# Performance work log

Measured on AMD Instinct MI355X. Metric: run time of the kernel, lower is better.

Reference implementation:

```python
import jax, jax.numpy as jnp
import numpy as np

D_MODEL = 1024
N_HEADS = 16
DH = D_MODEL // N_HEADS
ROPE_THETA = 10000.0


def rotate_half(u):
    h = u.shape[-1] // 2
    return jnp.concatenate([-u[..., h:], u[..., :h]], axis=-1)


def apply_rope(q, k, cos, sin):
    return q * cos + rotate_half(q) * sin, k * cos + rotate_half(k) * sin


def setup_inputs() -> dict:
    key = jax.random.key(0)
    ks = jax.random.split(key, 6)
    B, S = 2, 2048
    x = jax.random.normal(ks[0], (B, S, D_MODEL), dtype=jnp.float32)
    y = jax.random.normal(ks[1], (B, S, D_MODEL), dtype=jnp.float32)
    wq = 0.01 * jax.random.normal(ks[2], (D_MODEL, D_MODEL), dtype=jnp.float32)
    wk = 0.01 * jax.random.normal(ks[3], (D_MODEL, D_MODEL), dtype=jnp.float32)
    wv = 0.01 * jax.random.normal(ks[4], (D_MODEL, D_MODEL), dtype=jnp.float32)
    wo = 0.01 * jax.random.normal(ks[5], (D_MODEL, D_MODEL), dtype=jnp.float32)
    return {"x": x, "y": y, "wq": wq, "wk": wk, "wv": wv, "wo": wo}


def reference(x, y, wq, wk, wv, wo):
    B, S, D = x.shape
    past_length = 0  # default; kv_cache=None

    Q = x @ wq.T                      # (B,S,D)
    K = y                             # NOTE: K is y un-projected (as in source)
    V = y @ wv.T
    # K1 = x @ wk.T is computed in the source but immediately overwritten
    # by the buggy second apply_rope call -> wk is unused in the output.
    V1 = x @ wo.T

    def heads(t):
        return t.reshape(B, S, N_HEADS, DH).transpose(0, 2, 1, 3)  # (B,H,S,dh)

    q_h, k_h, v_h, v1_h = heads(Q), heads(K), heads(V), heads(V1)

    # RoPE tables (past_length:past_length+S rows of the cache)
    freqs = 1.0 / ROPE_THETA ** (jnp.arange(0, DH, 2, dtype=jnp.float32) / DH)
    emb = jnp.arange(past_length, past_length + S, dtype=jnp.float32)[:, None] * freqs[None, :]
    cos = jnp.concatenate([jnp.cos(emb), jnp.cos(emb)], axis=-1)[None, None]  # (1,1,S,dh)
    sin = jnp.concatenate([jnp.sin(emb), jnp.sin(emb)], axis=-1)[None, None]

    q_h, k_h = apply_rope(q_h, k_h, cos, sin)
    # faithful to source: k1 = rope applied AGAIN to the already-roped k
    _, k1_h = apply_rope(q_h, k_h, cos, sin)

    k_full = jnp.concatenate([k_h, k1_h], axis=2)   # (B,H,2S,dh)
    v_full = jnp.concatenate([v_h, v1_h], axis=2)
    S_full = k_full.shape[2]

    # mask: tril(diagonal=past_length) over (S,S_full), last S cols = eye(S)
    rows = jnp.arange(S)[:, None]
    cols = jnp.arange(S_full)[None, :]
    mask = cols <= rows + past_length
    mask = mask.at[:, -S:].set(jnp.eye(S, dtype=bool))  # (S,S_full)

    scores = jnp.einsum("bhqd,bhkd->bhqk", q_h, k_full) / jnp.sqrt(jnp.asarray(DH, x.dtype))
    scores = jnp.where(mask[None, None], scores, jnp.asarray(-1e30, x.dtype))
    attn = jax.nn.softmax(scores, axis=-1)
    out = jnp.einsum("bhqk,bhkd->bhqd", attn, v_full)
    out = out.transpose(0, 2, 1, 3).reshape(B, S, D)

    k_ret = k_full[:, :, :-S, :]
    return out, k_ret
```

## Files before the change

### kernel.cpp

```cpp
#include <hip/hip_runtime.h>

#define DM 1024
#define NHEADS 16
#define DHEAD 64
#define BB 2
#define SS 2048
#define BH (BB*NHEADS)

typedef __attribute__((ext_vector_type(8))) short short8;
typedef __attribute__((ext_vector_type(4))) float float4v;
typedef unsigned short ushort_t;

#define LN1E4_D32 0.28782313662425572f

static __device__ __forceinline__ unsigned short f2bf(float f) {
    union { float f; unsigned u; } v; v.f = f;
    unsigned r = v.u + 0x7fffu + ((v.u >> 16) & 1u);
    return (unsigned short)(r >> 16);
}
static __device__ __forceinline__ float bf2f(unsigned short u) {
    union { float f; unsigned u; } v; v.u = ((unsigned)u) << 16;
    return v.f;
}
static __device__ __forceinline__ unsigned cvtpk_bf16(float lo, float hi) {
    unsigned r;
    asm("v_cvt_pk_bf16_f32 %0, %1, %2" : "=v"(r) : "v"(lo), "v"(hi));
    return r;
}

static __device__ __forceinline__ void gload16(const ushort_t* g, ushort_t* l) {
    __builtin_amdgcn_global_load_lds(
        (const __attribute__((address_space(1))) void*)g,
        (__attribute__((address_space(3))) void*)l, 16, 0, 0);
}

__global__ __launch_bounds__(256) void prep_kernel(
        const float* __restrict__ x, const float* __restrict__ y,
        const float* __restrict__ wq, const float* __restrict__ wv,
        const float* __restrict__ wo,
        ushort_t* __restrict__ xb, ushort_t* __restrict__ wqb,
        ushort_t* __restrict__ wvb, ushort_t* __restrict__ wob,
        float* __restrict__ kout, ushort_t* __restrict__ khb,
        ushort_t* __restrict__ yb) {
    if (blockIdx.x < 3584) {
        int C = blockIdx.x * 256 + threadIdx.x;
        int c  = C & 511;
        int tl = C >> 9;
        int rb = tl >> 5, kb = tl & 31;
        const float* src; ushort_t* dst; int r0;
        if (rb < 32)      { src = x;  r0 = rb * 128;        dst = xb  + (size_t)tl * 4096; }
        else if (rb < 40) { src = wq; r0 = (rb - 32) * 128; dst = wqb + (size_t)(((rb - 32) * 32) + kb) * 4096; }
        else if (rb < 48) { src = wv; r0 = (rb - 40) * 128; dst = wvb + (size_t)(((rb - 40) * 32) + kb) * 4096; }
        else              { src = wo; r0 = (rb - 48) * 128; dst = wob + (size_t)(((rb - 48) * 32) + kb) * 4096; }
        int row = c >> 2, g = c & 3;
        int kk3 = g ^ ((row >> 1) & 3);
        const float* s = src + (size_t)(r0 + row) * DM + kb * 32 + kk3 * 8;
        float4 a0 = *reinterpret_cast<const float4*>(s);
        float4 a1 = *reinterpret_cast<const float4*>(s + 4);
        short8 v;
        v[0] = (short)f2bf(a0.x); v[1] = (short)f2bf(a0.y);
        v[2] = (short)f2bf(a0.z); v[3] = (short)f2bf(a0.w);
        v[4] = (short)f2bf(a1.x); v[5] = (short)f2bf(a1.y);
        v[6] = (short)f2bf(a1.z); v[7] = (short)f2bf(a1.w);
        *reinterpret_cast<short8*>(dst + c * 8) = v;
        return;
    }
    int t = (blockIdx.x - 3584) * 256 + threadIdx.x;
    int i8 = t & 3;
    int s  = (t >> 2) & (SS - 1);
    int bh = t >> 13;
    int h = bh & (NHEADS - 1), b = bh >> 4;

    const float* yp = y + ((size_t)(b * SS + s)) * DM + h * DHEAD + i8 * 8;
    float4 a0 = *reinterpret_cast<const float4*>(yp);
    float4 a1 = *reinterpret_cast<const float4*>(yp + 4);
    float4 b0 = *reinterpret_cast<const float4*>(yp + 32);
    float4 b1 = *reinterpret_cast<const float4*>(yp + 36);
    float u0[8] = {a0.x, a0.y, a0.z, a0.w, a1.x, a1.y, a1.z, a1.w};
    float u1[8] = {b0.x, b0.y, b0.z, b0.w, b1.x, b1.y, b1.z, b1.w};
    float lo[8], hi[8];
#pragma unroll
    for (int j = 0; j < 8; j++) {
        int i = i8 * 8 + j;
        float freq = __expf(-(float)i * LN1E4_D32);
        float th = (float)s * freq;
        float cv = cosf(th), sv = sinf(th);
        lo[j] = u0[j] * cv - u1[j] * sv;
        hi[j] = u1[j] * cv + u0[j] * sv;
    }
    float* op = kout + ((size_t)bh * SS + s) * DHEAD + i8 * 8;
    *reinterpret_cast<float4*>(op)      = (float4){lo[0], lo[1], lo[2], lo[3]};
    *reinterpret_cast<float4*>(op + 4)  = (float4){lo[4], lo[5], lo[6], lo[7]};
    *reinterpret_cast<float4*>(op + 32) = (float4){hi[0], hi[1], hi[2], hi[3]};
    *reinterpret_cast<float4*>(op + 36) = (float4){hi[4], hi[5], hi[6], hi[7]};

    ushort_t* kb = khb + ((size_t)bh * 32 + (s >> 6)) * 4096 + (s & 63) * 64;
    short8 vlo, vhi;
#pragma unroll
    for (int j = 0; j < 8; j++) { vlo[j] = (short)f2bf(lo[j]); vhi[j] = (short)f2bf(hi[j]); }
    *reinterpret_cast<short8*>(kb + ((i8 ^ (s & 7)) << 3))       = vlo;
    *reinterpret_cast<short8*>(kb + (((i8 + 4) ^ (s & 7)) << 3)) = vhi;

    int rowm = b * SS + s;
    int rowin = rowm & 127, rbm = rowm >> 7;
    int g = i8 ^ ((rowin >> 1) & 3);
    ushort_t* yt = yb + ((size_t)(rbm * 32 + h * 2)) * 4096 + rowin * 32 + (g << 3);
    short8 ulo, uhi;
#pragma unroll
    for (int j = 0; j < 8; j++) { ulo[j] = (short)f2bf(u0[j]); uhi[j] = (short)f2bf(u1[j]); }
    *reinterpret_cast<short8*>(yt)        = ulo;
    *reinterpret_cast<short8*>(yt + 4096) = uhi;
}

__global__ __launch_bounds__(256, 2) void gemm3_kernel(
        const ushort_t* __restrict__ xb, const ushort_t* __restrict__ yb,
        const ushort_t* __restrict__ wqb, const ushort_t* __restrict__ wvb,
        const ushort_t* __restrict__ wob,
        ushort_t* __restrict__ qh, ushort_t* __restrict__ vt, ushort_t* __restrict__ v1h) {
    __shared__ __align__(16) char smem[34816];
    ushort_t* As = (ushort_t*)smem;
    ushort_t* Bs = (ushort_t*)(smem + 16384);
    ushort_t (*Ct)[136] = (ushort_t(*)[136])smem;

    int bid = blockIdx.x;
    int xcd = bid & 7;
    int s_  = bid >> 3;
    int zo  = s_ >> 5;
    int z   = (zo == 0) ? 0 : (zo == 1 ? 2 : 1);
    int t_  = s_ & 31;
    int n0  = (t_ >> 2) * 128;
    int m0  = (xcd * 4 + (t_ & 3)) * 128;

    const ushort_t* A = (z == 1) ? yb : xb;
    const ushort_t* W = (z == 0) ? wqb : (z == 1 ? wvb : wob);
    ushort_t* O = (z == 0) ? qh : (z == 1 ? vt : v1h);

    const ushort_t* Atl = A + (size_t)(m0 >> 7) * 32 * 4096;
    const ushort_t* Wtl = W + (size_t)(n0 >> 7) * 32 * 4096;

    int tid = threadIdx.x;
    int wave = tid >> 6, lane = tid & 63, quad = lane >> 4, l15 = lane & 15;
    int wr = (wave >> 1) * 64, wc = (wave & 1) * 64;

    int gi0 = tid * 8, gi1 = (256 + tid) * 8;
    int li0 = (tid & 192) * 8, li1 = (256 + (tid & 192)) * 8;

    int aoff[4], boff[4];
#pragma unroll
    for (int mi = 0; mi < 4; mi++) {
        int row = wr + mi * 16 + l15;
        aoff[mi] = row * 32 + ((quad ^ ((row >> 1) & 3)) << 3);
    }
#pragma unroll
    for (int ni = 0; ni < 4; ni++) {
        int row = wc + ni * 16 + l15;
        boff[ni] = row * 32 + ((quad ^ ((row >> 1) & 3)) << 3);
    }

    float4v acc[4][4];
#pragma unroll
    for (int a = 0; a < 4; a++)
#pragma unroll
        for (int b = 0; b < 4; b++)
            acc[a][b] = (float4v){0.f, 0.f, 0.f, 0.f};

    gload16(Atl + gi0, As + li0); gload16(Atl + gi1, As + li1);
    gload16(Wtl + gi0, Bs + li0); gload16(Wtl + gi1, Bs + li1);
    int cur = 0;

    for (int kb = 0; kb < 32; kb++) {
        __syncthreads();
        if (kb + 1 < 32) {
            const ushort_t* at = Atl + (size_t)(kb + 1) * 4096;
            const ushort_t* wt = Wtl + (size_t)(kb + 1) * 4096;
            int nb = (cur ^ 1) * 4096;
            gload16(at + gi0, As + nb + li0); gload16(at + gi1, As + nb + li1);
            gload16(wt + gi0, Bs + nb + li0); gload16(wt + gi1, Bs + nb + li1);
        }
        const ushort_t* Ac = As + cur * 4096;
        const ushort_t* Bc = Bs + cur * 4096;
        short8 af[4], bfr[4];
#pragma unroll
        for (int mi = 0; mi < 4; mi++)
            af[mi] = *reinterpret_cast<const short8*>(&Ac[aoff[mi]]);
#pragma unroll
        for (int ni = 0; ni < 4; ni++)
            bfr[ni] = *reinterpret_cast<const short8*>(&Bc[boff[ni]]);
#pragma unroll
        for (int mi = 0; mi < 4; mi++)
#pragma unroll
            for (int ni = 0; ni < 4; ni++)
                acc[mi][ni] = __builtin_amdgcn_mfma_f32_16x16x32_bf16(af[mi], bfr[ni], acc[mi][ni], 0, 0, 0);
        cur ^= 1;
    }

    if (z == 0) {
#pragma unroll
        for (int mi = 0; mi < 4; mi++)
#pragma unroll
            for (int r = 0; r < 4; r++) {
                int m = m0 + wr + mi * 16 + quad * 4 + r;
                float pos = (float)(m & (SS - 1));
#pragma unroll
                for (int ni = 0; ni < 2; ni++) {
                    int d = ni * 16 + l15;
                    float f = __expf(-(float)d * LN1E4_D32);
                    float th = pos * f;
                    float cv, sv;
                    __sincosf(th, &sv, &cv);
                    float u0 = acc[mi][ni][r], u1 = acc[mi][ni + 2][r];
                    acc[mi][ni][r]     = u0 * cv - u1 * sv;
                    acc[mi][ni + 2][r] = u1 * cv + u0 * sv;
                }
            }
    }

    __syncthreads();
#pragma unroll
    for (int mi = 0; mi < 4; mi++)
#pragma unroll
        for (int ni = 0; ni < 4; ni++) {
            int col = wc + ni * 16 + l15;
#pragma unroll
            for (int r = 0; r < 4; r++)
                Ct[wr + mi * 16 + quad * 4 + r][col] = f2bf(acc[mi][ni][r]);
        }
    __syncthreads();
    int h0 = n0 >> 6;
    if (z == 1) {
        int b = m0 >> 11;
        int s0 = m0 & (SS - 1);
#pragma unroll
        for (int it = 0; it < 8; it++) {
            int c = it * 256 + tid;
            int dh  = c & 63;
            int k16 = (c >> 6) & 15;
            int hh  = c >> 10;
            short8 v;
#pragma unroll
            for (int e = 0; e < 8; e++)
                v[e] = (short)Ct[k16 * 8 + e][hh * 64 + dh];
            int kt = (s0 >> 6) + (k16 >> 3);
            size_t off = ((size_t)((b * NHEADS + h0 + hh) * 32 + kt)) * 4096
                       + dh * 64 + (((k16 & 7) ^ (dh & 7)) << 3);
            *reinterpret_cast<short8*>(&O[off]) = v;
        }
    } else {
#pragma unroll
        for (int it = 0; it < 8; it++) {
            int c = it * 256 + tid;
            int o = c >> 3, j = c & 7;
            int hh = o >> 7, mr = o & 127;
            int m = m0 + mr, b = m >> 11, si = m & (SS - 1);
            uint4 v = *reinterpret_cast<const uint4*>(&Ct[mr][hh * 64 + j * 8]);
            *reinterpret_cast<uint4*>(
                &O[((size_t)((b * NHEADS + h0 + hh) * SS + si)) * DHEAD + j * 8]) = v;
        }
    }
}

template<bool MASKED>
static __device__ __forceinline__ void attn_tile(
        const ushort_t* __restrict__ Kc, const ushort_t* __restrict__ Vc, int kbase,
        int quad, int l15, int q0w, const short8* qf,
        ushort_t* __restrict__ Psw, float4v* Oa, float& lsum) {
    float4v sa[4];
#pragma unroll
    for (int t2 = 0; t2 < 4; t2++) sa[t2] = (float4v){0.f, 0.f, 0.f, 0.f};
    __builtin_amdgcn_s_setprio(1);
#pragma unroll
    for (int t2 = 0; t2 < 4; t2++) {
        int key = t2 * 16 + l15;
        int ro = key * 64, sw = key & 7;
#pragma unroll
        for (int half = 0; half < 2; half++) {
            short8 kf = *reinterpret_cast<const short8*>(&Kc[ro + (((half * 4 + quad) ^ sw) << 3)]);
            sa[t2] = __builtin_amdgcn_mfma_f32_16x16x32_bf16(kf, qf[half], sa[t2], 0, 0, 0);
        }
    }
    __builtin_amdgcn_s_setprio(0);
    int query = q0w + l15;
    int swl = l15 & 7;
#pragma unroll
    for (int t2 = 0; t2 < 4; t2++) {
        float p[4];
#pragma unroll
        for (int r = 0; r < 4; r++) {
            float e = __expf(sa[t2][r] * 0.125f);
            if (MASKED) {
                int key = kbase + t2 * 16 + quad * 4 + r;
                p[r] = (key <= query) ? e : 0.f;
            } else {
                p[r] = e;
            }
        }
        lsum += (p[0] + p[1]) + (p[2] + p[3]);
        unsigned w0 = cvtpk_bf16(p[0], p[1]);
        unsigned w1 = cvtpk_bf16(p[2], p[3]);
        int chunk = (((t2 * 2 + (quad >> 1)) ^ swl) << 3) + (quad & 1) * 4;
        *reinterpret_cast<unsigned*>(&Psw[l15 * 64 + chunk])     = w0;
        *reinterpret_cast<unsigned*>(&Psw[l15 * 64 + chunk + 2]) = w1;
    }
    short8 pf0 = *reinterpret_cast<const short8*>(&Psw[l15 * 64 + ((quad ^ swl) << 3)]);
    short8 pf1 = *reinterpret_cast<const short8*>(&Psw[l15 * 64 + (((4 + quad) ^ swl) << 3)]);
    __builtin_amdgcn_s_setprio(1);
#pragma unroll
    for (int t = 0; t < 4; t++) {
        int dh = t * 16 + l15;
        int ro = dh * 64, sw = dh & 7;
        short8 vf0 = *reinterpret_cast<const short8*>(&Vc[ro + ((quad ^ sw) << 3)]);
        short8 vf1 = *reinterpret_cast<const short8*>(&Vc[ro + (((4 + quad) ^ sw) << 3)]);
        Oa[t] = __builtin_amdgcn_mfma_f32_16x16x32_bf16(pf0, vf0, Oa[t], 0, 0, 0);
        Oa[t] = __builtin_amdgcn_mfma_f32_16x16x32_bf16(pf1, vf1, Oa[t], 0, 0, 0);
    }
    __builtin_amdgcn_s_setprio(0);
}

__global__ __launch_bounds__(512, 4) void attn_kernel(
        const ushort_t* __restrict__ qh, const float* __restrict__ kf32,
        const ushort_t* __restrict__ khb, const ushort_t* __restrict__ vtb,
        const ushort_t* __restrict__ v1h, float* __restrict__ out) {
    __shared__ __align__(16) ushort_t Ks[2][4096];
    __shared__ __align__(16) ushort_t Vt[2][4096];
    __shared__ __align__(16) ushort_t Ps[8][1024];

    int bid = blockIdx.x;
    int bh = (bid & 7) * 4 + ((bid >> 3) & 3);
    int p  = bid >> 5;

    int tid = threadIdx.x, wave = tid >> 6, lane = tid & 63, quad = lane >> 4, l15 = lane & 15;
    int jq  = (wave < 4) ? p : (31 - p);
    int q0w = jq * 64 + (wave & 3) * 16;
    const ushort_t* qp  = qh  + (size_t)bh * SS * DHEAD;
    const float*    kp  = kf32 + (size_t)bh * SS * DHEAD;
    const ushort_t* v1p = v1h + (size_t)bh * SS * DHEAD;
    const ushort_t* ktb = khb + (size_t)bh * 32 * 4096;
    const ushort_t* vtt = vtb + (size_t)bh * 32 * 4096;

    short8 qf[2];
    qf[0] = *reinterpret_cast<const short8*>(&qp[(q0w + l15) * DHEAD + quad * 8]);
    qf[1] = *reinterpret_cast<const short8*>(&qp[(q0w + l15) * DHEAD + 32 + quad * 8]);

    float4v Oa[4];
#pragma unroll
    for (int t = 0; t < 4; t++) Oa[t] = (float4v){0.f, 0.f, 0.f, 0.f};
    float lsum = 0.f;

    int gi = tid * 8;
    int li = (tid & 448) * 8;

    int ntiles = 32 - p;
    gload16(ktb + gi, &Ks[0][li]);
    gload16(vtt + gi, &Vt[0][li]);
    int cur = 0;

    for (int kt = 0; kt < ntiles; kt++) {
        __syncthreads();
        if (kt + 1 < ntiles) {
            const ushort_t* gk = ktb + (size_t)(kt + 1) * 4096;
            const ushort_t* gv = vtt + (size_t)(kt + 1) * 4096;
            int nb = cur ^ 1;
            gload16(gk + gi, &Ks[nb][li]);
            gload16(gv + gi, &Vt[nb][li]);
        }
        int kbase = kt * 64;
        if (kbase <= q0w + 15) {
            if (kbase + 63 <= q0w)
                attn_tile<false>(Ks[cur], Vt[cur], kbase, quad, l15, q0w, qf,
                                 &Ps[wave][0], Oa, lsum);
            else
                attn_tile<true>(Ks[cur], Vt[cur], kbase, quad, l15, q0w, qf,
                                &Ps[wave][0], Oa, lsum);
        }
        cur ^= 1;
    }

    float* sred  = reinterpret_cast<float*>(&Ps[wave][0]);
    float* sdiag = reinterpret_cast<float*>(&Ps[wave][32]);

    lsum += __shfl_xor(lsum, 16);
    lsum += __shfl_xor(lsum, 32);
    if (quad == 0) sred[l15] = lsum;

    {
        int sk = q0w + l15;
        const float* krow = kp + (size_t)sk * DHEAD;
        short8 k1lo, k1hi;
#pragma unroll
        for (int j = 0; j < 8; j++) {
            int d = quad * 8 + j;
            float f = __expf(-(float)d * LN1E4_D32);
            float th = (float)sk * f;
            float cv, sv;
            __sincosf(th, &sv, &cv);
            float a = krow[d], b2 = krow[d + 32];
            k1lo[j] = (short)f2bf(a * cv - b2 * sv);
            k1hi[j] = (short)f2bf(b2 * cv + a * sv);
        }
        float4v sd4 = (float4v){0.f, 0.f, 0.f, 0.f};
        sd4 = __builtin_amdgcn_mfma_f32_16x16x32_bf16(qf[0], k1lo, sd4, 0, 0, 0);
        sd4 = __builtin_amdgcn_mfma_f32_16x16x32_bf16(qf[1], k1hi, sd4, 0, 0, 0);
#pragma unroll
        for (int r = 0; r < 4; r++)
            if (l15 == quad * 4 + r) sdiag[l15] = sd4[r] * 0.125f;
        __syncthreads();

        int b = bh >> 4, h = bh & (NHEADS - 1);
#pragma unroll
        for (int r = 0; r < 4; r++) {
            float ls = sred[quad * 4 + r];
            float pd = __expf(sdiag[quad * 4 + r]);
            int query = q0w + quad * 4 + r;
            float linv = 1.f / (ls + pd);
#pragma unroll
            for (int t = 0; t < 4; t++) {
                float v1v = bf2f(v1p[query * DHEAD + t * 16 + l15]);
                float o = (Oa[t][r] + pd * v1v) * linv;
                out[(b * SS + query) * DM + h * DHEAD + t * 16 + l15] = o;
            }
        }
    }
}

extern "C" void kernel_launch(void* const* d_in, const int* in_sizes, int n_in,
                              void* d_out, int out_size, void* d_ws, size_t ws_size,
                              hipStream_t stream) {
    const float* x  = (const float*)d_in[0];
    const float* y  = (const float*)d_in[1];
    const float* wq = (const float*)d_in[2];
    const float* wv = (const float*)d_in[4];
    const float* wo = (const float*)d_in[5];
    float* outp  = (float*)d_out;
    float* k_out = outp + (size_t)BB * SS * DM;

    char* ws = (char*)d_ws;
    ushort_t* vtb = (ushort_t*)(ws);
    ushort_t* v1b = (ushort_t*)(ws + (8ull  << 20));
    ushort_t* qhb = (ushort_t*)(ws + (16ull << 20));
    ushort_t* khb = (ushort_t*)(ws + (24ull << 20));
    ushort_t* xb  = (ushort_t*)(ws + (32ull << 20));
    ushort_t* yb  = (ushort_t*)(ws + (40ull << 20));
    ushort_t* wqb = (ushort_t*)(ws + (48ull << 20));
    ushort_t* wvb = (ushort_t*)(ws + (50ull << 20));
    ushort_t* wob = (ushort_t*)(ws + (52ull << 20));

    prep_kernel<<<4608, 256, 0, stream>>>(x, y, wq, wv, wo, xb, wqb, wvb, wob,
                                          k_out, khb, yb);
    gemm3_kernel<<<768, 256, 0, stream>>>(xb, yb, wqb, wvb, wob, qhb, vtb, v1b);
    attn_kernel<<<512, 512, 0, stream>>>(qhb, k_out, khb, vtb, v1b, outp);
}
```

Measured before the change: 168.9 us.

## Fold softmax scale into RoPE'd Q, use exp2, compute row sums via MFMA

Pre-multiplies Q by scale*log2(e) during the projection epilogue so the attention loop can call raw v_exp_f32 instead of __expf with a multiply. Replaces per-lane scalar row-sum accumulation and the final shuffle/LDS reduction with two extra MFMAs per tile against a ones vector, which also removes a __syncthreads. The row sum now comes from bf16-rounded probabilities, which matches what is multiplied into V, and the MFMA pipe takes on slightly more work. Removing the barrier relies on sdiag being written and read within a single wave.

```diff
diff --git a/kernel.cpp b/kernel.cpp
--- a/kernel.cpp
+++ b/kernel.cpp
@@ -12,6 +12,7 @@
 typedef unsigned short ushort_t;
 
 #define LN1E4_D32 0.28782313662425572f
+#define SM_SCALE  0.18033688011112042f
 
 static __device__ __forceinline__ unsigned short f2bf(float f) {
     union { float f; unsigned u; } v; v.f = f;
@@ -25,6 +26,11 @@
 static __device__ __forceinline__ unsigned cvtpk_bf16(float lo, float hi) {
     unsigned r;
     asm("v_cvt_pk_bf16_f32 %0, %1, %2" : "=v"(r) : "v"(lo), "v"(hi));
+    return r;
+}
+static __device__ __forceinline__ float ex2(float x) {
+    float r;
+    asm("v_exp_f32 %0, %1" : "=v"(r) : "v"(x));
     return r;
 }
 
@@ -208,6 +214,7 @@
                     float th = pos * f;
                     float cv, sv;
                     __sincosf(th, &sv, &cv);
+                    cv *= SM_SCALE; sv *= SM_SCALE;
                     float u0 = acc[mi][ni][r], u1 = acc[mi][ni + 2][r];
                     acc[mi][ni][r]     = u0 * cv - u1 * sv;
                     acc[mi][ni + 2][r] = u1 * cv + u0 * sv;
@@ -262,8 +269,8 @@
 template<bool MASKED>
 static __device__ __forceinline__ void attn_tile(
         const ushort_t* __restrict__ Kc, const ushort_t* __restrict__ Vc, int kbase,
-        int quad, int l15, int q0w, const short8* qf,
-        ushort_t* __restrict__ Psw, float4v* Oa, float& lsum) {
+        int quad, int l15, int q0w, const short8* qf, const short8& onesf,
+        ushort_t* __restrict__ Psw, float4v* Oa, float4v& sum4) {
     float4v sa[4];
 #pragma unroll
     for (int t2 = 0; t2 < 4; t2++) sa[t2] = (float4v){0.f, 0.f, 0.f, 0.f};
@@ -286,7 +293,7 @@
         float p[4];
 #pragma unroll
         for (int r = 0; r < 4; r++) {
-            float e = __expf(sa[t2][r] * 0.125f);
+            float e = ex2(sa[t2][r]);
             if (MASKED) {
                 int key = kbase + t2 * 16 + quad * 4 + r;
                 p[r] = (key <= query) ? e : 0.f;
@@ -294,7 +301,6 @@
                 p[r] = e;
             }
         }
-        lsum += (p[0] + p[1]) + (p[2] + p[3]);
         unsigned w0 = cvtpk_bf16(p[0], p[1]);
         unsigned w1 = cvtpk_bf16(p[2], p[3]);
         int chunk = (((t2 * 2 + (quad >> 1)) ^ swl) << 3) + (quad & 1) * 4;
@@ -313,6 +319,8 @@
         Oa[t] = __builtin_amdgcn_mfma_f32_16x16x32_bf16(pf0, vf0, Oa[t], 0, 0, 0);
         Oa[t] = __builtin_amdgcn_mfma_f32_16x16x32_bf16(pf1, vf1, Oa[t], 0, 0, 0);
     }
+    sum4 = __builtin_amdgcn_mfma_f32_16x16x32_bf16(pf0, onesf, sum4, 0, 0, 0);
+    sum4 = __builtin_amdgcn_mfma_f32_16x16x32_bf16(pf1, onesf, sum4, 0, 0, 0);
     __builtin_amdgcn_s_setprio(0);
 }
 
@@ -340,11 +348,14 @@
     short8 qf[2];
     qf[0] = *reinterpret_cast<const short8*>(&qp[(q0w + l15) * DHEAD + quad * 8]);
     qf[1] = *reinterpret_cast<const short8*>(&qp[(q0w + l15) * DHEAD + 32 + quad * 8]);
+    short8 onesf;
+#pragma unroll
+    for (int j = 0; j < 8; j++) onesf[j] = (short)0x3F80;
 
     float4v Oa[4];
 #pragma unroll
     for (int t = 0; t < 4; t++) Oa[t] = (float4v){0.f, 0.f, 0.f, 0.f};
-    float lsum = 0.f;
+    float4v sum4 = (float4v){0.f, 0.f, 0.f, 0.f};
 
     int gi = tid * 8;
     int li = (tid & 448) * 8;
@@ -366,21 +377,16 @@
         int kbase = kt * 64;
         if (kbase <= q0w + 15) {
             if (kbase + 63 <= q0w)
-                attn_tile<false>(Ks[cur], Vt[cur], kbase, quad, l15, q0w, qf,
-                                 &Ps[wave][0], Oa, lsum);
+                attn_tile<false>(Ks[cur], Vt[cur], kbase, quad, l15, q0w, qf, onesf,
+                                 &Ps[wave][0], Oa, sum4);
             else
-                attn_tile<true>(Ks[cur], Vt[cur], kbase, quad, l15, q0w, qf,
-                                &Ps[wave][0], Oa, lsum);
+                attn_tile<true>(Ks[cur], Vt[cur], kbase, quad, l15, q0w, qf, onesf,
+                                &Ps[wave][0], Oa, sum4);
         }
         cur ^= 1;
     }
 
-    float* sred  = reinterpret_cast<float*>(&Ps[wave][0]);
     float* sdiag = reinterpret_cast<float*>(&Ps[wave][32]);
-
-    lsum += __shfl_xor(lsum, 16);
-    lsum += __shfl_xor(lsum, 32);
-    if (quad == 0) sred[l15] = lsum;
 
     {
         int sk = q0w + l15;
@@ -402,16 +408,14 @@
         sd4 = __builtin_amdgcn_mfma_f32_16x16x32_bf16(qf[1], k1hi, sd4, 0, 0, 0);
 #pragma unroll
         for (int r = 0; r < 4; r++)
-            if (l15 == quad * 4 + r) sdiag[l15] = sd4[r] * 0.125f;
-        __syncthreads();
+            if (l15 == quad * 4 + r) sdiag[l15] = sd4[r];
 
         int b = bh >> 4, h = bh & (NHEADS - 1);
 #pragma unroll
         for (int r = 0; r < 4; r++) {
-            float ls = sred[quad * 4 + r];
-            float pd = __expf(sdiag[quad * 4 + r]);
+            float pd = ex2(sdiag[quad * 4 + r]);
             int query = q0w + quad * 4 + r;
-            float linv = 1.f / (ls + pd);
+            float linv = 1.f / (sum4[r] + pd);
 #pragma unroll
             for (int t = 0; t < 4; t++) {
                 float v1v = bf2f(v1p[query * DHEAD + t * 16 + l15]);
```

Result: no change. 168.3 us (-0.4%).
